# Kernel tuning notes

Hardware: AMD Instinct MI355X
Metric: run time of the kernel (lower is better)

The kernel has to match this reference:

```python
import jax, jax.numpy as jnp
import numpy as np

N_NODES = 50000
N_EDGES = 800000
N_GRAPHS = 1000
IN_F = 11
H = 128
BN_EPS = 1e-5


def _bn(h, g, b):
    # BatchNorm1d training-mode math (biased variance), no running stats
    m = h.mean(axis=0)
    v = h.var(axis=0)
    return (h - m) * jax.lax.rsqrt(v + BN_EPS) * g + b


def _mlp(h, w1, b1, g1, be1, w2, b2, g2, be2):
    h = jax.nn.relu(_bn(h @ w1 + b1, g1, be1))
    h = jax.nn.relu(_bn(h @ w2 + b2, g2, be2))
    return h


def _gin_agg(h, edge_index):
    # GINConv with eps=0: (1+eps)*x + sum_{j->i} x_j
    msgs = h[edge_index[0]]  # [E, F] gather
    agg = jax.ops.segment_sum(msgs, edge_index[1], num_segments=N_NODES)
    return h + agg


def setup_inputs() -> dict:
    key = jax.random.key(0)
    ks = jax.random.split(key, 24)
    d = {}
    d["x"] = jax.random.normal(ks[0], (N_NODES, IN_F), dtype=jnp.float32)
    d["edge_index"] = jax.random.randint(ks[1], (2, N_EDGES), 0, N_NODES, dtype=jnp.int64)
    d["batch"] = jnp.sort(jax.random.randint(ks[2], (N_NODES,), 0, N_GRAPHS, dtype=jnp.int64))

    dims = [
        ("l1", IN_F, H), ("l2", H, H),            # conv1 MLP
        ("l3", H, 2 * H), ("l4", 2 * H, 2 * H),    # conv2 MLP
        ("l5", 2 * H, 2 * H), ("l6", 2 * H, 2 * H),# conv3 MLP
    ]
    ki = 3
    for name, fi, fo in dims:
        d[name + "w"] = jax.random.normal(ks[ki], (fi, fo), dtype=jnp.float32) * (1.0 / np.sqrt(fi)); ki += 1
        d[name + "b"] = jax.random.normal(ks[ki], (fo,), dtype=jnp.float32) * 0.02; ki += 1
        d[name + "g"] = 1.0 + jax.random.normal(ks[ki], (fo,), dtype=jnp.float32) * 0.02; ki += 1
        d[name + "be"] = jax.random.normal(ks[ki], (fo,), dtype=jnp.float32) * 0.02; ki += 1
        ks = jax.random.split(ks[-1], 24); ki = 0
    d["fw1"] = jax.random.normal(ks[0], (2 * H, H), dtype=jnp.float32) * (1.0 / np.sqrt(2 * H))
    d["fb1"] = jax.random.normal(ks[1], (H,), dtype=jnp.float32) * 0.02
    d["fg"] = 1.0 + jax.random.normal(ks[2], (H,), dtype=jnp.float32) * 0.02
    d["fbe"] = jax.random.normal(ks[3], (H,), dtype=jnp.float32) * 0.02
    d["fw2"] = jax.random.normal(ks[4], (H, 1), dtype=jnp.float32) * (1.0 / np.sqrt(H))
    d["fb2"] = jax.random.normal(ks[5], (1,), dtype=jnp.float32) * 0.02
    return d


def reference(x, edge_index, batch,
              l1w, l1b, l1g, l1be, l2w, l2b, l2g, l2be,
              l3w, l3b, l3g, l3be, l4w, l4b, l4g, l4be,
              l5w, l5b, l5g, l5be, l6w, l6b, l6g, l6be,
              fw1, fb1, fg, fbe, fw2, fb2):
    # conv1 + relu (dropout = identity in eval)
    h = _mlp(_gin_agg(x, edge_index), l1w, l1b, l1g, l1be, l2w, l2b, l2g, l2be)
    h = jax.nn.relu(h)
    # conv2 + relu
    h = _mlp(_gin_agg(h, edge_index), l3w, l3b, l3g, l3be, l4w, l4b, l4g, l4be)
    h = jax.nn.relu(h)
    # conv3 + relu
    h = _mlp(_gin_agg(h, edge_index), l5w, l5b, l5g, l5be, l6w, l6b, l6g, l6be)
    h = jax.nn.relu(h)
    # global_add_pool over graphs
    hg = jax.ops.segment_sum(h, batch, num_segments=N_GRAPHS)  # [G, 256]
    hg = jax.nn.relu(_bn(hg @ fw1 + fb1, fg, fbe))
    out = hg @ fw2 + fb2  # [G, 1]
    return out.reshape(-1)
```

## Files before the change

### kernel.cpp

```cpp
#include <hip/hip_runtime.h>

#define NNODES 50000
#define NEDGES 800000
#define NGRAPHS 1000
#define BN_EPS 1e-5f
#define MPAD 50048

typedef unsigned short us_t;
typedef us_t us8 __attribute__((ext_vector_type(8)));
typedef us_t us4 __attribute__((ext_vector_type(4)));
typedef __bf16 bf16x8 __attribute__((ext_vector_type(8)));
typedef float f32x4 __attribute__((ext_vector_type(4)));

__device__ __forceinline__ float b2f(us_t u) {
    union { unsigned int i; float f; } v;
    v.i = ((unsigned int)u) << 16;
    return v.f;
}
__device__ __forceinline__ us_t f2b(float x) {
    unsigned int u = __float_as_uint(x);
    unsigned int r = u + 0x7FFFu + ((u >> 16) & 1u);
    return (us_t)(r >> 16);
}
__device__ __forceinline__ float h2f(us_t u) {
    _Float16 h;
    __builtin_memcpy(&h, &u, 2);
    return (float)h;
}
__device__ __forceinline__ us_t f2h(float x) {
    _Float16 h = (_Float16)x;
    us_t u;
    __builtin_memcpy(&u, &h, 2);
    return u;
}
__device__ __forceinline__ bf16x8 as_bf(us8 v) {
    union { us8 u; bf16x8 b; } c;
    c.u = v;
    return c.b;
}

__device__ __forceinline__ void glds16(const us_t* g, us_t* l) {
    __builtin_amdgcn_global_load_lds(
        (const __attribute__((address_space(1))) void*)g,
        (__attribute__((address_space(3))) void*)l, 16, 0, 0);
}


__global__ void zero_f32(float* __restrict__ p, int n) {
    int i = blockIdx.x * blockDim.x + threadIdx.x;
    if (i < n) p[i] = 0.f;
}


__global__ void csr_hist(const int* __restrict__ dst, int* __restrict__ deg, int E) {
    int e = blockIdx.x * blockDim.x + threadIdx.x;
    if (e < E) atomicAdd(&deg[dst[e]], 1);
}

__global__ void csr_scan1(const int* __restrict__ deg, int* __restrict__ tmpscan,
                          int* __restrict__ chunkTot, int n) {
    __shared__ int sm[1024];
    int i = blockIdx.x * 1024 + threadIdx.x;
    int v = (i < n) ? deg[i] : 0;
    sm[threadIdx.x] = v;
    __syncthreads();
    for (int off = 1; off < 1024; off <<= 1) {
        int add = (threadIdx.x >= off) ? sm[threadIdx.x - off] : 0;
        __syncthreads();
        sm[threadIdx.x] += add;
        __syncthreads();
    }
    if (i < n) tmpscan[i] = sm[threadIdx.x];
    if (threadIdx.x == 1023) chunkTot[blockIdx.x] = sm[1023];
}

__global__ void csr_scan2(int* __restrict__ chunkTot, int nchunks) {
    if (threadIdx.x == 0 && blockIdx.x == 0) {
        int run = 0;
        for (int c = 0; c < nchunks; c++) {
            int t = chunkTot[c];
            chunkTot[c] = run;
            run += t;
        }
    }
}

__global__ void csr_scan3(const int* __restrict__ deg, const int* __restrict__ tmpscan,
                          const int* __restrict__ chunkTot, int* __restrict__ rowptr,
                          int* __restrict__ cursor, int n) {
    int i = blockIdx.x * blockDim.x + threadIdx.x;
    if (i < n) {
        int inc = tmpscan[i] + chunkTot[i >> 10];
        rowptr[i + 1] = inc;
        cursor[i] = inc - deg[i];
        if (i == 0) rowptr[0] = 0;
    }
}

__global__ void csr_fill(const int* __restrict__ src, const int* __restrict__ dst,
                         int* __restrict__ cursor, int* __restrict__ eidx, int E) {
    int e = blockIdx.x * blockDim.x + threadIdx.x;
    if (e < E) {
        int pos = atomicAdd(&cursor[dst[e]], 1);
        eidx[pos] = src[e];
    }
}


__global__ void wt_convert_all(const float* __restrict__ w2, const float* __restrict__ w3,
                               const float* __restrict__ w4, const float* __restrict__ w5,
                               const float* __restrict__ w6,
                               us_t* __restrict__ o2, us_t* __restrict__ o3,
                               us_t* __restrict__ o4, us_t* __restrict__ o5,
                               us_t* __restrict__ o6) {
    int i = blockIdx.x * blockDim.x + threadIdx.x;
    if (i < 16384) {
        int k = i >> 7, n = i & 127;
        o2[n * 128 + k] = f2b(w2[i]);
    } else if (i < 49152) {
        int j = i - 16384; int k = j >> 8, n = j & 255;
        o3[n * 128 + k] = f2b(w3[j]);
    } else if (i < 114688) {
        int j = i - 49152; int k = j >> 8, n = j & 255;
        o4[n * 256 + k] = f2b(w4[j]);
    } else if (i < 180224) {
        int j = i - 114688; int k = j >> 8, n = j & 255;
        o5[n * 256 + k] = f2b(w5[j]);
    } else if (i < 245760) {
        int j = i - 180224; int k = j >> 8, n = j & 255;
        o6[n * 256 + k] = f2b(w6[j]);
    }
}


__global__ void gin_gather_bn128(const us_t* __restrict__ z, const float* __restrict__ sums,
                                 const float* __restrict__ sumsq, const float* __restrict__ gw,
                                 const float* __restrict__ bw, float invM,
                                 const int* __restrict__ rowptr, const int* __restrict__ eidx,
                                 us_t* __restrict__ out) {
    int ln = threadIdx.x >> 4;
    int fp = threadIdx.x & 15;
    int n = blockIdx.x * 16 + ln;
    if (n >= NNODES) return;
    int f0 = fp * 8;
    float s[8], t[8];
    #pragma unroll
    for (int q = 0; q < 8; q++) {
        float m = sums[f0 + q] * invM;
        float va = sumsq[f0 + q] * invM - m * m;
        s[q] = gw[f0 + q] * rsqrtf(va + BN_EPS);
        t[q] = bw[f0 + q] - m * s[q];
    }
    const us_t* zf = z + f0;
    float a[8];
    us8 v = *(const us8*)&zf[(size_t)n * 128];
    #pragma unroll
    for (int q = 0; q < 8; q++) a[q] = fmaxf(0.f, b2f(v[q]) * s[q] + t[q]);
    int p0 = rowptr[n], p1 = rowptr[n + 1];
    int p = p0;
    for (; p + 4 <= p1; p += 4) {
        int e0 = eidx[p], e1 = eidx[p + 1], e2 = eidx[p + 2], e3 = eidx[p + 3];
        us8 u0 = *(const us8*)&zf[(size_t)e0 * 128];
        us8 u1 = *(const us8*)&zf[(size_t)e1 * 128];
        us8 u2 = *(const us8*)&zf[(size_t)e2 * 128];
        us8 u3 = *(const us8*)&zf[(size_t)e3 * 128];
        #pragma unroll
        for (int q = 0; q < 8; q++)
            a[q] += fmaxf(0.f, b2f(u0[q]) * s[q] + t[q]) +
                    fmaxf(0.f, b2f(u1[q]) * s[q] + t[q]) +
                    fmaxf(0.f, b2f(u2[q]) * s[q] + t[q]) +
                    fmaxf(0.f, b2f(u3[q]) * s[q] + t[q]);
    }
    for (; p < p1; p++) {
        us8 u = *(const us8*)&zf[(size_t)eidx[p] * 128];
        #pragma unroll
        for (int q = 0; q < 8; q++) a[q] += fmaxf(0.f, b2f(u[q]) * s[q] + t[q]);
    }
    us8 o;
    #pragma unroll
    for (int q = 0; q < 8; q++) o[q] = f2b(a[q]);
    *(us8*)&out[(size_t)n * 128 + f0] = o;
}


__global__ void gin_gather_bn256(const us_t* __restrict__ z, const float* __restrict__ sums,
                                 const float* __restrict__ sumsq, const float* __restrict__ gw,
                                 const float* __restrict__ bw, float invM,
                                 const int* __restrict__ rowptr, const int* __restrict__ eidx,
                                 us_t* __restrict__ out) {
    int ln = threadIdx.x >> 5;
    int fp = threadIdx.x & 31;
    int n = blockIdx.x * 8 + ln;
    if (n >= NNODES) return;
    int f0 = fp * 8;
    float s[8], t[8];
    #pragma unroll
    for (int q = 0; q < 8; q++) {
        float m = sums[f0 + q] * invM;
        float va = sumsq[f0 + q] * invM - m * m;
        s[q] = gw[f0 + q] * rsqrtf(va + BN_EPS);
        t[q] = bw[f0 + q] - m * s[q];
    }
    const us_t* zf = z + f0;
    float a[8];
    us8 v = *(const us8*)&zf[(size_t)n * 256];
    #pragma unroll
    for (int q = 0; q < 8; q++) a[q] = fmaxf(0.f, b2f(v[q]) * s[q] + t[q]);
    int p0 = rowptr[n], p1 = rowptr[n + 1];
    int p = p0;
    for (; p + 4 <= p1; p += 4) {
        int e0 = eidx[p], e1 = eidx[p + 1], e2 = eidx[p + 2], e3 = eidx[p + 3];
        us8 u0 = *(const us8*)&zf[(size_t)e0 * 256];
        us8 u1 = *(const us8*)&zf[(size_t)e1 * 256];
        us8 u2 = *(const us8*)&zf[(size_t)e2 * 256];
        us8 u3 = *(const us8*)&zf[(size_t)e3 * 256];
        #pragma unroll
        for (int q = 0; q < 8; q++)
            a[q] += fmaxf(0.f, b2f(u0[q]) * s[q] + t[q]) +
                    fmaxf(0.f, b2f(u1[q]) * s[q] + t[q]) +
                    fmaxf(0.f, b2f(u2[q]) * s[q] + t[q]) +
                    fmaxf(0.f, b2f(u3[q]) * s[q] + t[q]);
    }
    for (; p < p1; p++) {
        us8 u = *(const us8*)&zf[(size_t)eidx[p] * 256];
        #pragma unroll
        for (int q = 0; q < 8; q++) a[q] += fmaxf(0.f, b2f(u[q]) * s[q] + t[q]);
    }
    us8 o;
    #pragma unroll
    for (int q = 0; q < 8; q++) o[q] = f2b(a[q]);
    *(us8*)&out[(size_t)n * 256 + f0] = o;
}

__global__ void gin_gather11(const float* __restrict__ x, const int* __restrict__ rowptr,
                             const int* __restrict__ eidx, float* __restrict__ out) {
    int local = threadIdx.x >> 4;
    int lane = threadIdx.x & 15;
    int n = blockIdx.x * 16 + local;
    if (n >= NNODES) return;
    int p0 = rowptr[n], p1 = rowptr[n + 1];
    float acc = (lane < 11) ? x[n * 11 + lane] : 0.f;
    for (int p = p0; p < p1; p++) {
        int src = eidx[p];
        if (lane < 11) acc += x[src * 11 + lane];
    }
    if (lane < 11) out[n * 11 + lane] = acc;
}


__global__ __launch_bounds__(256) void gemm11(const float* __restrict__ A,
                                              const float* __restrict__ W,
                                              const float* __restrict__ b,
                                              us_t* __restrict__ C,
                                              float* __restrict__ sums,
                                              float* __restrict__ sumsq) {
    __shared__ float sW[11 * 128];
    __shared__ float sArows[64 * 11];
    int tid = threadIdx.x;
    for (int i = tid; i < 11 * 128; i += 256) sW[i] = W[i];
    int r0 = blockIdx.x * 64;
    for (int i = tid; i < 64 * 11; i += 256) {
        int r = i / 11, c = i - r * 11;
        sArows[i] = (r0 + r < NNODES) ? A[(r0 + r) * 11 + c] : 0.f;
    }
    __syncthreads();
    int col = tid & 127;
    int half = tid >> 7;
    float bias = b[col];
    float cs = 0.f, cq = 0.f;
    for (int rr = half * 32; rr < half * 32 + 32; rr++) {
        int row = r0 + rr;
        if (row < NNODES) {
            float acc = bias;
            #pragma unroll
            for (int k = 0; k < 11; k++) acc += sArows[rr * 11 + k] * sW[k * 128 + col];
            C[(size_t)row * 128 + col] = f2h(acc);
            cs += acc;
            cq += acc * acc;
        }
    }
    __syncthreads();
    sArows[tid] = cs;
    sArows[256 + tid] = cq;
    __syncthreads();
    if (tid < 128) {
        atomicAdd(&sums[tid], sArows[tid] + sArows[tid + 128]);
        atomicAdd(&sumsq[tid], sArows[256 + tid] + sArows[256 + tid + 128]);
    }
}


template <int K_, int AMODE, int OMODE, int COLS>
__global__ __launch_bounds__(256, 4) void gemm_v8(
    const void* __restrict__ Ap, const us_t* __restrict__ Wt,
    const float* __restrict__ bias,
    const float* __restrict__ sums_in, const float* __restrict__ sumsq_in,
    const float* __restrict__ gma, const float* __restrict__ bet, float invM,
    us_t* __restrict__ Cp, float* __restrict__ sums, float* __restrict__ sumsq,
    int M, int N, int nrows) {
    __shared__ us_t sAB[2 * 128 * 32];
    __shared__ float sST[(AMODE >= 1) ? 2 * K_ : 2];
    us_t* sA = sAB;
    us_t* sB = sAB + 128 * 32;

    int rowblk, colblk;
    if (COLS == 1) {
        rowblk = blockIdx.x;
        colblk = 0;
    } else {
        int g = blockIdx.x;
        rowblk = (g >> 4) * 8 + (g & 7);
        colblk = (g >> 3) & 1;
        if (rowblk >= nrows) return;
    }
    const int bm = rowblk * 128;
    const int bn = colblk * 128;

    const int tid = threadIdx.x;
    const int lane = tid & 63;
    const int wave = tid >> 6;
    const int wm = wave >> 1, wn = wave & 1;
    const int lrow = lane & 15, lquad = lane >> 4;

    if (AMODE >= 1) {
        if (tid < K_) {
            float m = sums_in[tid] * invM;
            float va = sumsq_in[tid] * invM - m * m;
            float sc = gma[tid] * rsqrtf(va + BN_EPS);
            sST[tid] = sc;
            sST[K_ + tid] = bet[tid] - m * sc;
        }
        __syncthreads();
    }

    f32x4 acc[4][4] = {};

    const int r0c = tid >> 2, q0c = tid & 3;
    const int r1c = (tid + 256) >> 2, q1c = tid & 3;

    #pragma unroll
    for (int kt = 0; kt < K_ / 32; kt++) {
        const int k0 = kt * 32;

        us8 pk[2];
        if (AMODE >= 1) {
            #pragma unroll
            for (int i = 0; i < 2; i++) {
                int row = (i == 0) ? r0c : r1c;
                int kq = (i == 0) ? q0c : q1c;
                int kk = k0 + kq * 8;
                float v[8];
                if (AMODE == 1) {
                    const float* ar = &((const float*)Ap)[(size_t)(bm + row) * K_ + kk];
                    float4 v0 = *(const float4*)ar;
                    float4 v1 = *(const float4*)(ar + 4);
                    v[0] = v0.x; v[1] = v0.y; v[2] = v0.z; v[3] = v0.w;
                    v[4] = v1.x; v[5] = v1.y; v[6] = v1.z; v[7] = v1.w;
                } else {
                    us8 u = *(const us8*)&((const us_t*)Ap)[(size_t)(bm + row) * K_ + kk];
                    #pragma unroll
                    for (int q = 0; q < 8; q++) v[q] = h2f(u[q]);
                }
                float4 s0 = *(const float4*)&sST[kk];
                float4 s1 = *(const float4*)&sST[kk + 4];
                float4 t0 = *(const float4*)&sST[K_ + kk];
                float4 t1 = *(const float4*)&sST[K_ + kk + 4];
                us8 o;
                o[0] = f2b(fmaxf(0.f, v[0] * s0.x + t0.x));
                o[1] = f2b(fmaxf(0.f, v[1] * s0.y + t0.y));
                o[2] = f2b(fmaxf(0.f, v[2] * s0.z + t0.z));
                o[3] = f2b(fmaxf(0.f, v[3] * s0.w + t0.w));
                o[4] = f2b(fmaxf(0.f, v[4] * s1.x + t1.x));
                o[5] = f2b(fmaxf(0.f, v[5] * s1.y + t1.y));
                o[6] = f2b(fmaxf(0.f, v[6] * s1.z + t1.z));
                o[7] = f2b(fmaxf(0.f, v[7] * s1.w + t1.w));
                pk[i] = o;
            }
        }

        __syncthreads();

        {
            glds16(&Wt[(size_t)(bn + r0c) * K_ + k0 + q0c * 8], &sB[(wave * 64) * 8]);
            glds16(&Wt[(size_t)(bn + r1c) * K_ + k0 + q1c * 8], &sB[(256 + wave * 64) * 8]);
        }
        if (AMODE == 0) {
            const us_t* A = (const us_t*)Ap;
            glds16(&A[(size_t)(bm + r0c) * K_ + k0 + q0c * 8], &sA[(wave * 64) * 8]);
            glds16(&A[(size_t)(bm + r1c) * K_ + k0 + q1c * 8], &sA[(256 + wave * 64) * 8]);
        } else {
            *(us8*)&sA[(size_t)tid * 8] = pk[0];
            *(us8*)&sA[(size_t)(tid + 256) * 8] = pk[1];
        }

        __syncthreads();

        bf16x8 af[4], bfr[4];
        #pragma unroll
        for (int i = 0; i < 4; i++)
            af[i] = as_bf(*(const us8*)&sA[(wm * 64 + i * 16 + lrow) * 32 + lquad * 8]);
        #pragma unroll
        for (int j = 0; j < 4; j++)
            bfr[j] = as_bf(*(const us8*)&sB[(wn * 64 + j * 16 + lrow) * 32 + lquad * 8]);
        #pragma unroll
        for (int i = 0; i < 4; i++)
            #pragma unroll
            for (int j = 0; j < 4; j++)
                acc[i][j] = __builtin_amdgcn_mfma_f32_16x16x32_bf16(af[i], bfr[j],
                                                                    acc[i][j], 0, 0, 0);
    }

    #pragma unroll
    for (int j = 0; j < 4; j++) {
        int col = bn + wn * 64 + j * 16 + lrow;
        float bcol = bias[col];
        float cs = 0.f, cq = 0.f;
        #pragma unroll
        for (int i = 0; i < 4; i++) {
            int rb = bm + wm * 64 + i * 16 + lquad * 4;
            #pragma unroll
            for (int r = 0; r < 4; r++) {
                if (rb + r < M) {
                    float zv = acc[i][j][r] + bcol;
                    cs += zv;
                    cq += zv * zv;
                }
            }
        }
        cs += __shfl_xor(cs, 16); cs += __shfl_xor(cs, 32);
        cq += __shfl_xor(cq, 16); cq += __shfl_xor(cq, 32);
        if (lquad == 0) {
            atomicAdd(&sums[col], cs);
            atomicAdd(&sumsq[col], cq);
        }
    }

    #pragma unroll
    for (int p = 0; p < 2; p++) {
        __syncthreads();
        if (wm == p) {
            #pragma unroll
            for (int j = 0; j < 4; j++) {
                int coll = wn * 64 + j * 16 + lrow;
                float bcol = bias[bn + coll];
                #pragma unroll
                for (int i = 0; i < 4; i++) {
                    int rl = i * 16 + lquad * 4;
                    #pragma unroll
                    for (int r = 0; r < 4; r++) {
                        float zv = acc[i][j][r] + bcol;
                        sAB[(rl + r) * 128 + coll] = (OMODE == 0) ? f2b(zv) : f2h(zv);
                    }
                }
            }
        }
        __syncthreads();
        #pragma unroll
        for (int k = 0; k < 4; k++) {
            int c = tid + 256 * k;
            int row = c >> 4, cw = c & 15;
            int grow = bm + p * 64 + row;
            if (grow < M)
                *(us8*)&Cp[(size_t)grow * N + bn + cw * 8] =
                    *(const us8*)&sAB[row * 128 + cw * 8];
        }
    }
}


__global__ void pool_bn_h(const us_t* __restrict__ z, const float* __restrict__ sums,
                          const float* __restrict__ sumsq, const float* __restrict__ gw,
                          const float* __restrict__ bw, float invM,
                          const int* __restrict__ batch, float* __restrict__ hg) {
    int f = threadIdx.x;
    float m = sums[f] * invM;
    float va = sumsq[f] * invM - m * m;
    float sv = gw[f] * rsqrtf(va + BN_EPS);
    float tv = bw[f] - m * sv;
    int n0 = blockIdx.x * 32;
    int n1 = min(n0 + 32, NNODES);
    float acc = 0.f;
    int gc = batch[n0];
    for (int n = n0; n < n1; n++) {
        int g = batch[n];
        if (g != gc) {
            atomicAdd(&hg[gc * 256 + f], acc);
            acc = 0.f;
            gc = g;
        }
        acc += fmaxf(0.f, h2f(z[(size_t)n * 256 + f]) * sv + tv);
    }
    atomicAdd(&hg[gc * 256 + f], acc);
}


#define GBM 128
#define GBN 128
#define GBK 16
#define LDA 132

__global__ __launch_bounds__(256) void gemm_f32_head(
    const float* __restrict__ A, const float* __restrict__ W, const float* __restrict__ bias,
    float* __restrict__ C, float* __restrict__ sums, float* __restrict__ sumsq,
    int M, int K, int N) {
    __shared__ float smem[2 * GBK * LDA];
    float* As = smem;
    float* Ws = smem + GBK * LDA;

    const int bm = blockIdx.y * GBM;
    const int bn = blockIdx.x * GBN;
    const int tid = threadIdx.x;
    const int tm = tid >> 4;
    const int tn = tid & 15;

    float acc[2][2][4][4] = {};

    for (int k0 = 0; k0 < K; k0 += GBK) {
        #pragma unroll
        for (int i = 0; i < 2; i++) {
            int id = tid + 256 * i;
            int row = id >> 2;
            int kq = id & 3;
            int gr = bm + row;
            int kk = k0 + kq * 4;
            float4 a4 = make_float4(0.f, 0.f, 0.f, 0.f);
            if (gr < M && kk < K) a4 = *(const float4*)&A[(size_t)gr * K + kk];
            As[(kq * 4 + 0) * LDA + row] = a4.x;
            As[(kq * 4 + 1) * LDA + row] = a4.y;
            As[(kq * 4 + 2) * LDA + row] = a4.z;
            As[(kq * 4 + 3) * LDA + row] = a4.w;
        }
        #pragma unroll
        for (int i = 0; i < 2; i++) {
            int id = tid + 256 * i;
            int kl = id >> 5;
            int c = id & 31;
            int kk = k0 + kl;
            float4 w4 = make_float4(0.f, 0.f, 0.f, 0.f);
            if (kk < K && bn + c * 4 < N) w4 = *(const float4*)&W[(size_t)kk * N + bn + c * 4];
            *(float4*)&Ws[kl * LDA + c * 4] = w4;
        }
        __syncthreads();
        #pragma unroll
        for (int k = 0; k < GBK; k++) {
            float4 a0 = *(float4*)&As[k * LDA + tm * 4];
            float4 a1 = *(float4*)&As[k * LDA + 64 + tm * 4];
            float4 w0 = *(float4*)&Ws[k * LDA + tn * 4];
            float4 w1 = *(float4*)&Ws[k * LDA + 64 + tn * 4];
            float ar[2][4] = {{a0.x, a0.y, a0.z, a0.w}, {a1.x, a1.y, a1.z, a1.w}};
            float wr[2][4] = {{w0.x, w0.y, w0.z, w0.w}, {w1.x, w1.y, w1.z, w1.w}};
            #pragma unroll
            for (int ri = 0; ri < 2; ri++)
                #pragma unroll
                for (int ci = 0; ci < 2; ci++)
                    #pragma unroll
                    for (int ii = 0; ii < 4; ii++)
                        #pragma unroll
                        for (int jj = 0; jj < 4; jj++)
                            acc[ri][ci][ii][jj] += ar[ri][ii] * wr[ci][jj];
        }
        __syncthreads();
    }

    float colsum[2][4] = {};
    float colsq[2][4] = {};
    #pragma unroll
    for (int ci = 0; ci < 2; ci++) {
        int colbase = bn + ci * 64 + tn * 4;
        if (colbase >= N) continue;
        float4 b4 = *(const float4*)&bias[colbase];
        float br[4] = {b4.x, b4.y, b4.z, b4.w};
        #pragma unroll
        for (int ri = 0; ri < 2; ri++) {
            #pragma unroll
            for (int ii = 0; ii < 4; ii++) {
                int row = bm + ri * 64 + tm * 4 + ii;
                if (row < M) {
                    float z0 = acc[ri][ci][ii][0] + br[0];
                    float z1 = acc[ri][ci][ii][1] + br[1];
                    float z2 = acc[ri][ci][ii][2] + br[2];
                    float z3 = acc[ri][ci][ii][3] + br[3];
                    *(float4*)&C[(size_t)row * N + colbase] = make_float4(z0, z1, z2, z3);
                    colsum[ci][0] += z0; colsq[ci][0] += z0 * z0;
                    colsum[ci][1] += z1; colsq[ci][1] += z1 * z1;
                    colsum[ci][2] += z2; colsq[ci][2] += z2 * z2;
                    colsum[ci][3] += z3; colsq[ci][3] += z3 * z3;
                }
            }
        }
    }
    __syncthreads();
    float* ps = smem;
    float* pq = smem + 2048;
    #pragma unroll
    for (int ci = 0; ci < 2; ci++)
        #pragma unroll
        for (int jj = 0; jj < 4; jj++) {
            int cl = ci * 64 + tn * 4 + jj;
            ps[tm * 128 + cl] = colsum[ci][jj];
            pq[tm * 128 + cl] = colsq[ci][jj];
        }
    __syncthreads();
    if (tid < 128 && bn + tid < N) {
        float s = 0.f, q = 0.f;
        #pragma unroll
        for (int i = 0; i < 16; i++) {
            s += ps[i * 128 + tid];
            q += pq[i * 128 + tid];
        }
        atomicAdd(&sums[bn + tid], s);
        atomicAdd(&sumsq[bn + tid], q);
    }
}


__global__ void final_gemv_raw(const float* __restrict__ hg2, const float* __restrict__ sums,
                               const float* __restrict__ sumsq, const float* __restrict__ gw,
                               const float* __restrict__ bw, float invM,
                               const float* __restrict__ fw2, const float* __restrict__ fb2,
                               float* __restrict__ out) {
    int g = blockIdx.x;
    int l = threadIdx.x;
    float m0 = sums[l] * invM, va0 = sumsq[l] * invM - m0 * m0;
    float s0 = gw[l] * rsqrtf(va0 + BN_EPS), t0 = bw[l] - m0 * s0;
    float m1 = sums[64 + l] * invM, va1 = sumsq[64 + l] * invM - m1 * m1;
    float s1 = gw[64 + l] * rsqrtf(va1 + BN_EPS), t1 = bw[64 + l] - m1 * s1;
    float a0 = fmaxf(0.f, hg2[g * 128 + l] * s0 + t0) * fw2[l];
    float a1 = fmaxf(0.f, hg2[g * 128 + 64 + l] * s1 + t1) * fw2[64 + l];
    float v = a0 + a1;
    #pragma unroll
    for (int o = 32; o > 0; o >>= 1) v += __shfl_down(v, o);
    if (l == 0) out[g] = v + fb2[0];
}


extern "C" void kernel_launch(void* const* d_in, const int* in_sizes, int n_in,
                              void* d_out, int out_size, void* d_ws, size_t ws_size,
                              hipStream_t stream) {
    const float* x = (const float*)d_in[0];
    const int* ei = (const int*)d_in[1];
    const int* batch = (const int*)d_in[2];
    const int* esrc = ei;
    const int* edst = ei + NEDGES;

    const float* l1w = (const float*)d_in[3],  *l1b = (const float*)d_in[4],
               * l1g = (const float*)d_in[5],  *l1be = (const float*)d_in[6];
    const float* l2w = (const float*)d_in[7],  *l2b = (const float*)d_in[8],
               * l2g = (const float*)d_in[9],  *l2be = (const float*)d_in[10];
    const float* l3w = (const float*)d_in[11], *l3b = (const float*)d_in[12],
               * l3g = (const float*)d_in[13], *l3be = (const float*)d_in[14];
    const float* l4w = (const float*)d_in[15], *l4b = (const float*)d_in[16],
               * l4g = (const float*)d_in[17], *l4be = (const float*)d_in[18];
    const float* l5w = (const float*)d_in[19], *l5b = (const float*)d_in[20],
               * l5g = (const float*)d_in[21], *l5be = (const float*)d_in[22];
    const float* l6w = (const float*)d_in[23], *l6b = (const float*)d_in[24],
               * l6g = (const float*)d_in[25], *l6be = (const float*)d_in[26];
    const float* fw1 = (const float*)d_in[27], *fb1 = (const float*)d_in[28],
               * fg  = (const float*)d_in[29], *fbe = (const float*)d_in[30];
    const float* fw2 = (const float*)d_in[31], *fb2 = (const float*)d_in[32];

    us_t* F0h = (us_t*)d_ws;
    us_t* Ba = F0h + (size_t)MPAD * 256;
    us_t* Bz = Ba + (size_t)MPAD * 256;
    us_t* wt2 = Bz + (size_t)MPAD * 256;
    us_t* wt3 = wt2 + 128 * 128;
    us_t* wt4 = wt3 + 256 * 128;
    us_t* wt5 = wt4 + 256 * 256;
    us_t* wt6 = wt5 + 256 * 256;
    float* agg11 = (float*)(wt6 + 256 * 256);
    float* hg = agg11 + (size_t)NNODES * 11;
    float* hg2 = hg + NGRAPHS * 256;
    float* stats = hg2 + NGRAPHS * 128;
    int* deg = (int*)(stats + 7 * 512);
    int* rowptr = deg + (NNODES + 1);
    int* cursor = rowptr + (NNODES + 1);
    int* chunkTot = cursor + (NNODES + 1);
    int* tmpscan = chunkTot + 64;
    int* eidx = tmpscan + (NNODES + 1);

    {
        int zn = NGRAPHS * 256 + NGRAPHS * 128 + 7 * 512 + (NNODES + 1);
        zero_f32<<<(zn + 255) / 256, 256, 0, stream>>>(hg, zn);
    }

    csr_hist<<<(NEDGES + 255) / 256, 256, 0, stream>>>(edst, deg, NEDGES);
    int nchunks = (NNODES + 1023) / 1024;
    csr_scan1<<<nchunks, 1024, 0, stream>>>(deg, tmpscan, chunkTot, NNODES);
    csr_scan2<<<1, 64, 0, stream>>>(chunkTot, nchunks);
    csr_scan3<<<(NNODES + 255) / 256, 256, 0, stream>>>(deg, tmpscan, chunkTot, rowptr,
                                                        cursor, NNODES);
    csr_fill<<<(NEDGES + 255) / 256, 256, 0, stream>>>(esrc, edst, cursor, eidx, NEDGES);

    wt_convert_all<<<(245760 + 255) / 256, 256, 0, stream>>>(l2w, l3w, l4w, l5w, l6w,
                                                             wt2, wt3, wt4, wt5, wt6);

    auto st = [&](int i) { return stats + i * 512; };
    const float invN = 1.0f / (float)NNODES;
    const float invG = 1.0f / (float)NGRAPHS;
    const int NRB = MPAD / 128;
    const int NSWZ = ((NRB + 7) / 8) * 16;

    gin_gather11<<<(NNODES + 15) / 16, 256, 0, stream>>>(x, rowptr, eidx, agg11);
    gemm11<<<(NNODES + 63) / 64, 256, 0, stream>>>(agg11, l1w, l1b, F0h, st(0), st(0) + 256);
    gemm_v8<128, 2, 0, 1><<<NRB, 256, 0, stream>>>(
        F0h, wt2, l2b, st(0), st(0) + 256, l1g, l1be, invN,
        Bz, st(1), st(1) + 256, NNODES, 128, NRB);

    gin_gather_bn128<<<(NNODES + 15) / 16, 256, 0, stream>>>(
        Bz, st(1), st(1) + 256, l2g, l2be, invN, rowptr, eidx, Ba);
    gemm_v8<128, 0, 2, 2><<<NSWZ, 256, 0, stream>>>(
        Ba, wt3, l3b, nullptr, nullptr, nullptr, nullptr, 0.f,
        F0h, st(2), st(2) + 256, NNODES, 256, NRB);
    gemm_v8<256, 2, 0, 2><<<NSWZ, 256, 0, stream>>>(
        F0h, wt4, l4b, st(2), st(2) + 256, l3g, l3be, invN,
        Bz, st(3), st(3) + 256, NNODES, 256, NRB);

    gin_gather_bn256<<<(NNODES + 7) / 8, 256, 0, stream>>>(
        Bz, st(3), st(3) + 256, l4g, l4be, invN, rowptr, eidx, Ba);
    gemm_v8<256, 0, 2, 2><<<NSWZ, 256, 0, stream>>>(
        Ba, wt5, l5b, nullptr, nullptr, nullptr, nullptr, 0.f,
        F0h, st(4), st(4) + 256, NNODES, 256, NRB);
    gemm_v8<256, 2, 2, 2><<<NSWZ, 256, 0, stream>>>(
        F0h, wt6, l6b, st(4), st(4) + 256, l5g, l5be, invN,
        Bz, st(5), st(5) + 256, NNODES, 256, NRB);

    pool_bn_h<<<(NNODES + 31) / 32, 256, 0, stream>>>(
        Bz, st(5), st(5) + 256, l6g, l6be, invN, batch, hg);
    gemm_f32_head<<<dim3(1, 8), 256, 0, stream>>>(hg, fw1, fb1, hg2, st(6), st(6) + 256,
                                                  NGRAPHS, 256, 128);
    final_gemv_raw<<<NGRAPHS, 64, 0, stream>>>(hg2, st(6), st(6) + 256, fg, fbe, invG,
                                               fw2, fb2, (float*)d_out);
}
```

Before: 600.7 us.

## Double-buffer GEMM shared-memory tiles to overlap loads with MFMA compute

The GEMM kernel now uses two shared-memory tile buffers. The next K-slice's weight and activation loads, plus the register prefetch of raw A values for the BN-fused mode, are issued before the MFMAs on the current slice, and each iteration needs one barrier instead of two. The BN+ReLU transform for the next slice runs after the MFMAs, and the output staging stride is padded to 136 to reduce LDS bank conflicts. Shared memory use doubles to 32KB per block, which may limit occupancy at 4 blocks per CU. The AMODE==1 fp32 path is dropped; it was unused.

```diff
diff --git a/kernel.cpp b/kernel.cpp
--- a/kernel.cpp
+++ b/kernel.cpp
@@ -291,17 +291,15 @@
 
 
 template <int K_, int AMODE, int OMODE, int COLS>
-__global__ __launch_bounds__(256, 4) void gemm_v8(
+__global__ __launch_bounds__(256, 4) void gemm_v10(
     const void* __restrict__ Ap, const us_t* __restrict__ Wt,
     const float* __restrict__ bias,
     const float* __restrict__ sums_in, const float* __restrict__ sumsq_in,
     const float* __restrict__ gma, const float* __restrict__ bet, float invM,
     us_t* __restrict__ Cp, float* __restrict__ sums, float* __restrict__ sumsq,
     int M, int N, int nrows) {
-    __shared__ us_t sAB[2 * 128 * 32];
-    __shared__ float sST[(AMODE >= 1) ? 2 * K_ : 2];
-    us_t* sA = sAB;
-    us_t* sB = sAB + 128 * 32;
+    __shared__ us_t smem[16384];
+    __shared__ float sST[(AMODE == 2) ? 2 * K_ : 2];
 
     int rowblk, colblk;
     if (COLS == 1) {
@@ -322,7 +320,7 @@
     const int wm = wave >> 1, wn = wave & 1;
     const int lrow = lane & 15, lquad = lane >> 4;
 
-    if (AMODE >= 1) {
+    if (AMODE == 2) {
         if (tid < K_) {
             float m = sums_in[tid] * invM;
             float va = sumsq_in[tid] * invM - m * m;
@@ -337,64 +335,65 @@
 
     const int r0c = tid >> 2, q0c = tid & 3;
     const int r1c = (tid + 256) >> 2, q1c = tid & 3;
-
-    #pragma unroll
-    for (int kt = 0; kt < K_ / 32; kt++) {
+    constexpr int NK = K_ / 32;
+
+    auto stage_glds = [&](int kt, us_t* tb) {
+        us_t* sBb = tb + 4096;
         const int k0 = kt * 32;
-
-        us8 pk[2];
-        if (AMODE >= 1) {
-            #pragma unroll
-            for (int i = 0; i < 2; i++) {
-                int row = (i == 0) ? r0c : r1c;
-                int kq = (i == 0) ? q0c : q1c;
-                int kk = k0 + kq * 8;
-                float v[8];
-                if (AMODE == 1) {
-                    const float* ar = &((const float*)Ap)[(size_t)(bm + row) * K_ + kk];
-                    float4 v0 = *(const float4*)ar;
-                    float4 v1 = *(const float4*)(ar + 4);
-                    v[0] = v0.x; v[1] = v0.y; v[2] = v0.z; v[3] = v0.w;
-                    v[4] = v1.x; v[5] = v1.y; v[6] = v1.z; v[7] = v1.w;
-                } else {
-                    us8 u = *(const us8*)&((const us_t*)Ap)[(size_t)(bm + row) * K_ + kk];
-                    #pragma unroll
-                    for (int q = 0; q < 8; q++) v[q] = h2f(u[q]);
-                }
-                float4 s0 = *(const float4*)&sST[kk];
-                float4 s1 = *(const float4*)&sST[kk + 4];
-                float4 t0 = *(const float4*)&sST[K_ + kk];
-                float4 t1 = *(const float4*)&sST[K_ + kk + 4];
-                us8 o;
-                o[0] = f2b(fmaxf(0.f, v[0] * s0.x + t0.x));
-                o[1] = f2b(fmaxf(0.f, v[1] * s0.y + t0.y));
-                o[2] = f2b(fmaxf(0.f, v[2] * s0.z + t0.z));
-                o[3] = f2b(fmaxf(0.f, v[3] * s0.w + t0.w));
-                o[4] = f2b(fmaxf(0.f, v[4] * s1.x + t1.x));
-                o[5] = f2b(fmaxf(0.f, v[5] * s1.y + t1.y));
-                o[6] = f2b(fmaxf(0.f, v[6] * s1.z + t1.z));
-                o[7] = f2b(fmaxf(0.f, v[7] * s1.w + t1.w));
-                pk[i] = o;
-            }
-        }
-
-        __syncthreads();
-
-        {
-            glds16(&Wt[(size_t)(bn + r0c) * K_ + k0 + q0c * 8], &sB[(wave * 64) * 8]);
-            glds16(&Wt[(size_t)(bn + r1c) * K_ + k0 + q1c * 8], &sB[(256 + wave * 64) * 8]);
-        }
+        glds16(&Wt[(size_t)(bn + r0c) * K_ + k0 + q0c * 8], &sBb[(wave * 64) * 8]);
+        glds16(&Wt[(size_t)(bn + r1c) * K_ + k0 + q1c * 8], &sBb[(256 + wave * 64) * 8]);
         if (AMODE == 0) {
             const us_t* A = (const us_t*)Ap;
-            glds16(&A[(size_t)(bm + r0c) * K_ + k0 + q0c * 8], &sA[(wave * 64) * 8]);
-            glds16(&A[(size_t)(bm + r1c) * K_ + k0 + q1c * 8], &sA[(256 + wave * 64) * 8]);
-        } else {
-            *(us8*)&sA[(size_t)tid * 8] = pk[0];
-            *(us8*)&sA[(size_t)(tid + 256) * 8] = pk[1];
-        }
-
-        __syncthreads();
-
+            glds16(&A[(size_t)(bm + r0c) * K_ + k0 + q0c * 8], &tb[(wave * 64) * 8]);
+            glds16(&A[(size_t)(bm + r1c) * K_ + k0 + q1c * 8], &tb[(256 + wave * 64) * 8]);
+        }
+    };
+    auto load_raw = [&](int kt, us8* raw) {
+        const us_t* A = (const us_t*)Ap;
+        const int k0 = kt * 32;
+        raw[0] = *(const us8*)&A[(size_t)(bm + r0c) * K_ + k0 + q0c * 8];
+        raw[1] = *(const us8*)&A[(size_t)(bm + r1c) * K_ + k0 + q1c * 8];
+    };
+    auto xform_write = [&](int kt, const us8* raw, us_t* tb) {
+        const int k0 = kt * 32;
+        #pragma unroll
+        for (int i = 0; i < 2; i++) {
+            int kk = k0 + ((i == 0) ? q0c : q1c) * 8;
+            float4 s0 = *(const float4*)&sST[kk];
+            float4 s1 = *(const float4*)&sST[kk + 4];
+            float4 t0 = *(const float4*)&sST[K_ + kk];
+            float4 t1 = *(const float4*)&sST[K_ + kk + 4];
+            us8 o;
+            o[0] = f2b(fmaxf(0.f, h2f(raw[i][0]) * s0.x + t0.x));
+            o[1] = f2b(fmaxf(0.f, h2f(raw[i][1]) * s0.y + t0.y));
+            o[2] = f2b(fmaxf(0.f, h2f(raw[i][2]) * s0.z + t0.z));
+            o[3] = f2b(fmaxf(0.f, h2f(raw[i][3]) * s0.w + t0.w));
+            o[4] = f2b(fmaxf(0.f, h2f(raw[i][4]) * s1.x + t1.x));
+            o[5] = f2b(fmaxf(0.f, h2f(raw[i][5]) * s1.y + t1.y));
+            o[6] = f2b(fmaxf(0.f, h2f(raw[i][6]) * s1.z + t1.z));
+            o[7] = f2b(fmaxf(0.f, h2f(raw[i][7]) * s1.w + t1.w));
+            *(us8*)&tb[(size_t)((i == 0) ? tid : (tid + 256)) * 8] = o;
+        }
+    };
+
+    stage_glds(0, smem);
+    us8 raw[2];
+    if (AMODE == 2) {
+        load_raw(0, raw);
+        xform_write(0, raw, smem);
+    }
+    __syncthreads();
+
+    #pragma unroll
+    for (int kt = 0; kt < NK; kt++) {
+        us_t* cur = smem + ((kt & 1) ? 8192 : 0);
+        us_t* nxt = smem + ((kt & 1) ? 0 : 8192);
+        if (kt + 1 < NK) {
+            stage_glds(kt + 1, nxt);
+            if (AMODE == 2) load_raw(kt + 1, raw);
+        }
+        us_t* sA = cur;
+        us_t* sB = cur + 4096;
         bf16x8 af[4], bfr[4];
         #pragma unroll
         for (int i = 0; i < 4; i++)
@@ -408,6 +407,8 @@
             for (int j = 0; j < 4; j++)
                 acc[i][j] = __builtin_amdgcn_mfma_f32_16x16x32_bf16(af[i], bfr[j],
                                                                     acc[i][j], 0, 0, 0);
+        if (AMODE == 2 && kt + 1 < NK) xform_write(kt + 1, raw, nxt);
+        __syncthreads();
     }
 
     #pragma unroll
@@ -449,7 +450,7 @@
                     #pragma unroll
                     for (int r = 0; r < 4; r++) {
                         float zv = acc[i][j][r] + bcol;
-                        sAB[(rl + r) * 128 + coll] = (OMODE == 0) ? f2b(zv) : f2h(zv);
+                        smem[(rl + r) * 136 + coll] = (OMODE == 0) ? f2b(zv) : f2h(zv);
                     }
                 }
             }
@@ -462,7 +463,7 @@
             int grow = bm + p * 64 + row;
             if (grow < M)
                 *(us8*)&Cp[(size_t)grow * N + bn + cw * 8] =
-                    *(const us8*)&sAB[row * 128 + cw * 8];
+                    *(const us8*)&smem[row * 136 + cw * 8];
         }
     }
 }
@@ -702,25 +703,25 @@
 
     gin_gather11<<<(NNODES + 15) / 16, 256, 0, stream>>>(x, rowptr, eidx, agg11);
     gemm11<<<(NNODES + 63) / 64, 256, 0, stream>>>(agg11, l1w, l1b, F0h, st(0), st(0) + 256);
-    gemm_v8<128, 2, 0, 1><<<NRB, 256, 0, stream>>>(
+    gemm_v10<128, 2, 0, 1><<<NRB, 256, 0, stream>>>(
         F0h, wt2, l2b, st(0), st(0) + 256, l1g, l1be, invN,
         Bz, st(1), st(1) + 256, NNODES, 128, NRB);
 
     gin_gather_bn128<<<(NNODES + 15) / 16, 256, 0, stream>>>(
         Bz, st(1), st(1) + 256, l2g, l2be, invN, rowptr, eidx, Ba);
-    gemm_v8<128, 0, 2, 2><<<NSWZ, 256, 0, stream>>>(
+    gemm_v10<128, 0, 2, 2><<<NSWZ, 256, 0, stream>>>(
         Ba, wt3, l3b, nullptr, nullptr, nullptr, nullptr, 0.f,
         F0h, st(2), st(2) + 256, NNODES, 256, NRB);
-    gemm_v8<256, 2, 0, 2><<<NSWZ, 256, 0, stream>>>(
+    gemm_v10<256, 2, 0, 2><<<NSWZ, 256, 0, stream>>>(
         F0h, wt4, l4b, st(2), st(2) + 256, l3g, l3be, invN,
         Bz, st(3), st(3) + 256, NNODES, 256, NRB);
 
     gin_gather_bn256<<<(NNODES + 7) / 8, 256, 0, stream>>>(
         Bz, st(3), st(3) + 256, l4g, l4be, invN, rowptr, eidx, Ba);
-    gemm_v8<256, 0, 2, 2><<<NSWZ, 256, 0, stream>>>(
+    gemm_v10<256, 0, 2, 2><<<NSWZ, 256, 0, stream>>>(
         Ba, wt5, l5b, nullptr, nullptr, nullptr, nullptr, 0.f,
         F0h, st(4), st(4) + 256, NNODES, 256, NRB);
-    gemm_v8<256, 2, 2, 2><<<NSWZ, 256, 0, stream>>>(
+    gemm_v10<256, 2, 2, 2><<<NSWZ, 256, 0, stream>>>(
         F0h, wt6, l6b, st(4), st(4) + 256, l5g, l5be, invN,
         Bz, st(5), st(5) + 256, NNODES, 256, NRB);
 
```

Result: no change. 605.3 us (+0.8%).
